# Kernel tuning notes

Measured on AMD Instinct MI355X. Metric: run time of the kernel, lower is better.

Reference implementation:

```python
import jax, jax.numpy as jnp
import numpy as np

B, N, M, D, H = 2, 256, 64, 768, 12
HD = D // H  # head dim 64


def setup_inputs() -> dict:
    key = jax.random.key(0)
    ks = jax.random.split(key, 8)
    s = 0.02
    return {
        "x": jax.random.normal(ks[0], (B, N, D), jnp.float32),
        "sim_embeddings": jax.random.normal(ks[1], (B, N, M, D), jnp.float32),
        "Wq": jax.random.normal(ks[2], (D, D), jnp.float32) * s,
        "bq": jnp.zeros((D,), jnp.float32),
        "Wkv": jax.random.normal(ks[3], (D, 2 * D), jnp.float32) * s,
        "bkv": jnp.zeros((2 * D,), jnp.float32),
        "Wp": jax.random.normal(ks[4], (D, D), jnp.float32) * s,
        "bp": jnp.zeros((D,), jnp.float32),
    }


def reference(x, sim_embeddings, Wq, bq, Wkv, bkv, Wp, bp):
    # x: (B,N,D); sim_embeddings: (B,N,M,D)
    b, n, d = x.shape
    m = sim_embeddings.shape[2]
    scale = HD ** -0.5

    q = (x @ Wq + bq).reshape(b, n, H, HD).transpose(0, 2, 1, 3)  # (B,H,N,hd)

    kv_x = x @ Wkv + bkv                       # (B,N,2D)
    k_x, v_x = jnp.split(kv_x, 2, axis=-1)
    k_x = k_x.reshape(b, n, H, HD).transpose(0, 2, 1, 3)  # (B,H,N,hd) shared-global K
    v_x = v_x.reshape(b, n, H, HD).transpose(0, 2, 1, 3)

    kv_s = sim_embeddings @ Wkv + bkv          # (B,N,M,2D)
    k_s, v_s = jnp.split(kv_s, 2, axis=-1)
    k_s = k_s.reshape(b, n, m, H, HD).transpose(0, 3, 1, 2, 4)  # (B,H,N,M,hd) per-query local K
    v_s = v_s.reshape(b, n, m, H, HD).transpose(0, 3, 1, 2, 4)

    # scores over concatenated [global N keys | local M keys] without expanding K to (B,N,N+M,D)
    sg = jnp.einsum('bhnd,bhkd->bhnk', q, k_x) * scale   # (B,H,N,N)
    sl = jnp.einsum('bhnd,bhnmd->bhnm', q, k_s) * scale  # (B,H,N,M)
    attn = jax.nn.softmax(jnp.concatenate([sg, sl], axis=-1), axis=-1)
    ag, al = attn[..., :n], attn[..., n:]

    out = (jnp.einsum('bhnk,bhkd->bhnd', ag, v_x)
           + jnp.einsum('bhnm,bhnmd->bhnd', al, v_s))   # (B,H,N,hd)
    out = out.transpose(0, 2, 1, 3).reshape(b, n, d)
    return out @ Wp + bp
```

## Files before the change

kernel.cpp:

```cpp
#include <hip/hip_runtime.h>
#include <stdint.h>

#define DEV_INLINE __device__ __forceinline__

typedef __bf16 bf16x8 __attribute__((ext_vector_type(8)));
typedef float f32x4 __attribute__((ext_vector_type(4)));

typedef const __attribute__((address_space(1))) void* gas_ptr;
typedef __attribute__((address_space(3))) void* las_ptr;

DEV_INLINE unsigned short f2bf(float f) {
    union { __bf16 h; unsigned short u; } v;
    v.h = (__bf16)f;
    return v.u;
}

template <int N> DEV_INLINE void waitcnt_vm() {
    asm volatile("s_waitcnt vmcnt(%0)" :: "n"(N) : "memory");
}
DEV_INLINE void hard_barrier() {
    __builtin_amdgcn_sched_barrier(0);
    __builtin_amdgcn_s_barrier();
    __builtin_amdgcn_sched_barrier(0);
}

__global__ __launch_bounds__(256)
void prep_all_kernel(const float* __restrict__ x, unsigned short* __restrict__ xb,
                     const float* __restrict__ Wkv, unsigned short* __restrict__ wkvb,
                     const float* __restrict__ bq, const float* __restrict__ bkv,
                     float* __restrict__ bias1, float* __restrict__ zbuf,
                     const float* __restrict__ Wq, const float* __restrict__ Wp,
                     unsigned short* __restrict__ w1t, unsigned short* __restrict__ wpt) {
    __shared__ float tl[64][65];
    const int bid = blockIdx.x, t = threadIdx.x;
    if (bid < 1536) {
        const float* s; unsigned short* d; long i;
        if (bid < 384) { s = x;   d = xb;   i = (long)bid * 256 + t; }
        else           { s = Wkv; d = wkvb; i = (long)(bid - 384) * 256 + t; }
        float4 a = ((const float4*)s)[i];
        ushort4 o;
        o.x = f2bf(a.x); o.y = f2bf(a.y); o.z = f2bf(a.z); o.w = f2bf(a.w);
        ((ushort4*)d)[i] = o;
    } else if (bid < 1548) {
        int i = (bid - 1536) * 256 + t;
        if (i < 768) bias1[i] = bq[i];
        else if (i < 2304) bias1[i] = bkv[i - 768];
        else zbuf[i - 2304] = 0.f;
    } else {
        int tb = bid - 1548;
        int bx = tb % 48, by = tb / 48;
        const float* src; unsigned short* dst; int C;
        if (bx < 12)      { src = Wq;  dst = w1t;              C = 768; }
        else if (bx < 36) { src = Wkv; dst = w1t + 768L * 768; C = 1536; bx -= 12; }
        else              { src = Wp;  dst = wpt;              C = 768; bx -= 36; }
        int c0 = bx * 64, r0 = by * 64;
        int tx = t & 63, ty = t >> 6;
        #pragma unroll
        for (int i = 0; i < 64; i += 4)
            tl[ty + i][tx] = src[(long)(r0 + ty + i) * C + c0 + tx];
        __syncthreads();
        #pragma unroll
        for (int i = 0; i < 64; i += 4)
            dst[(long)(c0 + ty + i) * 768 + r0 + tx] = f2bf(tl[tx][ty + i]);
    }
}

template <int WM, int WN, int WAVES_M, bool G1E>
DEV_INLINE void gemm_body(const unsigned short* A, int lda,
                          const unsigned short* BT, int ldb,
                          const unsigned short* A2, int lda2,
                          const unsigned short* B2, int ldb2, int K1,
                          const float* bias, void* Cout, int ldc, int K,
                          const float* cin, int OUT, long obase, long tm, long tn,
                          unsigned short* As, unsigned short* Bs,
                          float* g1_qf, unsigned short* g1_qb,
                          unsigned short* g1_kxb, unsigned short* g1_vxT) {
    constexpr int TR = WAVES_M * WM * 16;
    constexpr int TC = (4 / WAVES_M) * WN * 16;
    constexpr int NL = TR / 32 + TC / 32;
    const int tid = threadIdx.x;
    const int w = tid >> 6, lane = tid & 63;
    const int lm = lane & 15, quad = lane >> 4;
    const int m_off = (w % WAVES_M) * WM * 16;
    const int n_off = (w / WAVES_M) * WN * 16;
    const int lrow8 = lane >> 3;
    const int lcol_sw = (((lane & 7) ^ lrow8) * 8);

    f32x4 acc[WM][WN];
    #pragma unroll
    for (int mi = 0; mi < WM; ++mi)
        #pragma unroll
        for (int ni = 0; ni < WN; ++ni) acc[mi][ni] = f32x4{0.f, 0.f, 0.f, 0.f};

    auto stage = [&](int k0, int pb) {
        const unsigned short* Ab; const unsigned short* Bb;
        int la, lb, kc;
        if (k0 < K1) { Ab = A;  Bb = BT; la = lda;  lb = ldb;  kc = k0; }
        else         { Ab = A2; Bb = B2; la = lda2; lb = ldb2; kc = k0 - K1; }
        unsigned short* Asb = As + pb * (TR * 64);
        unsigned short* Bsb = Bs + pb * (TC * 64);
        #pragma unroll
        for (int i = 0; i < TR / 32; ++i) {
            int rr = w * (TR / 4) + i * 8;
            const unsigned short* ga = Ab + (tm + rr + lrow8) * la + kc + lcol_sw;
            __builtin_amdgcn_global_load_lds((gas_ptr)ga, (las_ptr)(Asb + rr * 64), 16, 0, 0);
        }
        #pragma unroll
        for (int i = 0; i < TC / 32; ++i) {
            int rr = w * (TC / 4) + i * 8;
            const unsigned short* gb = Bb + (tn + rr + lrow8) * lb + kc + lcol_sw;
            __builtin_amdgcn_global_load_lds((gas_ptr)gb, (las_ptr)(Bsb + rr * 64), 16, 0, 0);
        }
    };

    stage(0, 0);
    const int nt = K >> 6;
    for (int t = 0; t < nt; ++t) {
        const int cur = t & 1;
        if (t + 1 < nt) {
            stage((t + 1) << 6, cur ^ 1);
            waitcnt_vm<NL>();
        } else {
            waitcnt_vm<0>();
        }
        hard_barrier();
        const unsigned short* Asb = As + cur * (TR * 64);
        const unsigned short* Bsb = Bs + cur * (TC * 64);
        #pragma unroll
        for (int kk = 0; kk < 2; ++kk) {
            bf16x8 af[WM], bfr[WN];
            #pragma unroll
            for (int mi = 0; mi < WM; ++mi) {
                int r = m_off + mi * 16 + lm;
                af[mi] = *(const bf16x8*)(Asb + r * 64 + (((kk * 4 + quad) ^ (r & 7)) * 8));
            }
            #pragma unroll
            for (int ni = 0; ni < WN; ++ni) {
                int r = n_off + ni * 16 + lm;
                bfr[ni] = *(const bf16x8*)(Bsb + r * 64 + (((kk * 4 + quad) ^ (r & 7)) * 8));
            }
            #pragma unroll
            for (int mi = 0; mi < WM; ++mi)
                #pragma unroll
                for (int ni = 0; ni < WN; ++ni)
                    acc[mi][ni] = __builtin_amdgcn_mfma_f32_16x16x32_bf16(
                        af[mi], bfr[ni], acc[mi][ni], 0, 0, 0);
        }
        hard_barrier();
    }

    #pragma unroll
    for (int mi = 0; mi < WM; ++mi) {
        #pragma unroll
        for (int ni = 0; ni < WN; ++ni) {
            long col = tn + n_off + ni * 16 + lm;
            float bv = bias[col];
            #pragma unroll
            for (int r = 0; r < 4; ++r) {
                long row = tm + m_off + mi * 16 + quad * 4 + r;
                float v = acc[mi][ni][r] + bv;
                if (G1E) {
                    if (col < 768) {
                        g1_qf[row * 768 + col] = v;
                        g1_qb[row * 768 + col] = f2bf(v);
                    } else if (col < 1536) {
                        g1_kxb[row * 768 + (col - 768)] = f2bf(v);
                    } else {
                        int j = (int)col - 1536, h = j >> 6, d = j & 63;
                        int bb = (int)row >> 8, nn = (int)row & 255;
                        g1_vxT[((long)(bb * 12 + h) * 64 + d) * 256 + nn] = f2bf(v);
                    }
                } else {
                    long idx = obase + row * ldc + col;
                    if (cin) v += cin[idx];
                    if (OUT == 0) ((float*)Cout)[idx] = v;
                    else ((unsigned short*)Cout)[idx] = f2bf(v);
                }
            }
        }
    }
}

template <int WM, int WN, int WAVES_M, bool G1E>
__global__ __launch_bounds__(256)
void gemm_bf16_kernel(const unsigned short* __restrict__ A, int lda,
                      const unsigned short* __restrict__ BT, int ldb,
                      const float* __restrict__ bias,
                      void* __restrict__ Cout, int ldc, int K,
                      const float* __restrict__ cin, int OUT,
                      long aZb, long aZh, long bZb, long bZh, long oZb, long oZh,
                      float* __restrict__ g1_qf, unsigned short* __restrict__ g1_qb,
                      unsigned short* __restrict__ g1_kxb,
                      unsigned short* __restrict__ g1_vxT) {
    constexpr int TR = WAVES_M * WM * 16;
    constexpr int TC = (4 / WAVES_M) * WN * 16;
    __shared__ unsigned short As[2 * TR * 64];
    __shared__ unsigned short Bs[2 * TC * 64];
    const int z = blockIdx.z, zb = z / 12, zh = z % 12;
    gemm_body<WM, WN, WAVES_M, G1E>(
        A + zb * aZb + zh * aZh, lda, BT + zb * bZb + zh * bZh, ldb,
        nullptr, 0, nullptr, 0, 1 << 30,
        bias, Cout, ldc, K, cin, OUT, zb * oZb + zh * oZh,
        (long)blockIdx.y * TR, (long)blockIdx.x * TC, As, Bs,
        g1_qf, g1_qb, g1_kxb, g1_vxT);
}

__global__ __launch_bounds__(256)
void gemm_qwsg_kernel(const unsigned short* __restrict__ qb,
                      const unsigned short* __restrict__ wkvb,
                      const unsigned short* __restrict__ kxb,
                      const float* __restrict__ zbuf,
                      unsigned short* __restrict__ qWb,
                      float* __restrict__ sgbuf) {
    __shared__ unsigned short As[2 * 64 * 64];
    __shared__ unsigned short Bs[2 * 64 * 64];
    int bid = blockIdx.x;
    if (bid < 1152) {
        int bx = bid % 12, by = (bid / 12) % 8, h = bid / 96;
        gemm_body<2, 2, 2, false>(
            qb + h * 64, 768, wkvb + h * 64, 1536,
            nullptr, 0, nullptr, 0, 1 << 30,
            zbuf, qWb, 768, 64, nullptr, 1, (long)h * 393216,
            (long)by * 64, (long)bx * 64, As, Bs,
            nullptr, nullptr, nullptr, nullptr);
    } else {
        int bid2 = bid - 1152;
        int bx = bid2 % 4, by = (bid2 / 4) % 4, z = bid2 / 16;
        int zb = z / 12, zh = z % 12;
        gemm_body<2, 2, 2, false>(
            qb + zb * 196608 + zh * 64, 768, kxb + zb * 196608 + zh * 64, 768,
            nullptr, 0, nullptr, 0, 1 << 30,
            zbuf, sgbuf, 256, 64, nullptr, 0,
            (long)zb * 786432 + (long)zh * 65536,
            (long)by * 64, (long)bx * 64, As, Bs,
            nullptr, nullptr, nullptr, nullptr);
    }
}

template <int WM, int WN, int WAVES_M>
__global__ __launch_bounds__(256)
void gemm_concat_kernel(const unsigned short* __restrict__ A, int lda, long aZb, long aZh,
                        const unsigned short* __restrict__ BT, int ldb, long bZb, long bZh,
                        const unsigned short* __restrict__ A2, int lda2, long a2Zb, long a2Zh,
                        const unsigned short* __restrict__ B2, int ldb2, long b2Zb, long b2Zh,
                        int K1, int K, const float* __restrict__ bias,
                        void* __restrict__ Cout, int ldc,
                        const float* __restrict__ cin, int OUT, long oZb, long oZh) {
    constexpr int TR = WAVES_M * WM * 16;
    constexpr int TC = (4 / WAVES_M) * WN * 16;
    __shared__ unsigned short As[2 * TR * 64];
    __shared__ unsigned short Bs[2 * TC * 64];
    const int z = blockIdx.z, zb = z / 12, zh = z % 12;
    gemm_body<WM, WN, WAVES_M, false>(
        A + zb * aZb + zh * aZh, lda, BT + zb * bZb + zh * bZh, ldb,
        A2 + zb * a2Zb + zh * a2Zh, lda2, B2 + zb * b2Zb + zh * b2Zh, ldb2, K1,
        bias, Cout, ldc, K, cin, OUT, zb * oZb + zh * oZh,
        (long)blockIdx.y * TR, (long)blockIdx.x * TC, As, Bs,
        nullptr, nullptr, nullptr, nullptr);
}

__global__ __launch_bounds__(512)
void attn_mega_kernel(const float* __restrict__ sim,
                      const unsigned short* __restrict__ qWb,
                      const float* __restrict__ qf,
                      const float* __restrict__ bkv,
                      const float* __restrict__ sgbuf,
                      unsigned short* __restrict__ agb,
                      float* __restrict__ outg0,
                      unsigned short* __restrict__ simbar) {
    __shared__ unsigned short sim_s[12 * 64 * 64];
    __shared__ unsigned short qw_s[16 * 784];
    __shared__ float scl[2][12][68];
    __shared__ float al_s[12][64];
    __shared__ float slb_s[12];

    const int t = threadIdx.x;
    const int lane = t & 63, w = t >> 6;
    const int lm = lane & 15, quad = lane >> 4;
    const int n_ = blockIdx.x;
    const int b = n_ >> 8, n = n_ & 255;
    const float* simn = sim + (long)n_ * 49152;

    #pragma unroll
    for (int g3 = 0; g3 < 3; ++g3) {
        float4 va[4], vb[4]; int dso[4];
        #pragma unroll
        for (int i = 0; i < 4; ++i) {
            int j = t + 512 * (g3 * 4 + i);
            int r = j / 96, rem = j - r * 96;
            int c = rem >> 3, q8 = rem & 7;
            const float* gp = simn + r * 768 + c * 64 + q8 * 8;
            va[i] = *(const float4*)gp;
            vb[i] = *(const float4*)(gp + 4);
            dso[i] = c * 4096 + r * 64 + ((q8 ^ (r & 7)) * 8);
        }
        #pragma unroll
        for (int i = 0; i < 4; ++i) {
            union { bf16x8 v; unsigned short u[8]; } pk;
            pk.u[0] = f2bf(va[i].x); pk.u[1] = f2bf(va[i].y);
            pk.u[2] = f2bf(va[i].z); pk.u[3] = f2bf(va[i].w);
            pk.u[4] = f2bf(vb[i].x); pk.u[5] = f2bf(vb[i].y);
            pk.u[6] = f2bf(vb[i].z); pk.u[7] = f2bf(vb[i].w);
            *(bf16x8*)(sim_s + dso[i]) = pk.v;
        }
    }

    #pragma unroll
    for (int rep = 0; rep < 2; ++rep) {
        int i = t + rep * 512;
        int h = i / 96, cc = i - h * 96;
        *(bf16x8*)(qw_s + h * 784 + cc * 8) =
            *(const bf16x8*)(qWb + ((long)h * 512 + n_) * 768 + cc * 8);
    }
    if (t < 128) {
        int i = t + 1024;
        int h = i / 96, cc = i - h * 96;
        *(bf16x8*)(qw_s + h * 784 + cc * 8) =
            *(const bf16x8*)(qWb + ((long)h * 512 + n_) * 768 + cc * 8);
    }
    if (t < 392) *(bf16x8*)(qw_s + 12 * 784 + t * 8) = bf16x8{};

    if (t < 256) {
        float p0 = qf[(long)n_ * 768 + t] * bkv[t];
        float p1 = qf[(long)n_ * 768 + t + 256] * bkv[t + 256];
        float p2 = qf[(long)n_ * 768 + t + 512] * bkv[t + 512];
        #pragma unroll
        for (int off = 32; off > 0; off >>= 1) {
            p0 += __shfl_xor(p0, off);
            p1 += __shfl_xor(p1, off);
            p2 += __shfl_xor(p2, off);
        }
        if (lane == 0) { slb_s[w] = p0; slb_s[w + 4] = p1; slb_s[w + 8] = p2; }
    }
    __syncthreads();

    {
        const int mb = w & 3, kh = w >> 2;
        f32x4 acc = {};
        const int r = mb * 16 + lm;
        #pragma unroll
        for (int cc = 0; cc < 6; ++cc) {
            const int c = kh * 6 + cc;
            #pragma unroll
            for (int kk = 0; kk < 2; ++kk) {
                bf16x8 af = *(const bf16x8*)(sim_s + c * 4096 + r * 64 +
                                             (((kk * 4 + quad) ^ (r & 7)) * 8));
                bf16x8 bfr = *(const bf16x8*)(qw_s + lm * 784 + c * 64 + kk * 32 + quad * 8);
                acc = __builtin_amdgcn_mfma_f32_16x16x32_bf16(af, bfr, acc, 0, 0, 0);
            }
        }
        if (lm < 12) {
            #pragma unroll
            for (int r2 = 0; r2 < 4; ++r2)
                scl[kh][lm][mb * 16 + quad * 4 + r2] = acc[r2];
        }
    }
    __syncthreads();

    if (w < 6) {
        #pragma unroll
        for (int i = 0; i < 2; ++i) {
            const int h = w * 2 + i;
            const float* sgr = sgbuf + (long)(b * 12 + h) * 65536 + (long)n * 256;
            float v0 = sgr[lane] * 0.125f, v1 = sgr[lane + 64] * 0.125f,
                  v2 = sgr[lane + 128] * 0.125f, v3 = sgr[lane + 192] * 0.125f;
            float v4 = (scl[0][h][lane] + scl[1][h][lane] + slb_s[h]) * 0.125f;
            float mx = fmaxf(fmaxf(fmaxf(v0, v1), fmaxf(v2, v3)), v4);
            #pragma unroll
            for (int off = 32; off > 0; off >>= 1) mx = fmaxf(mx, __shfl_xor(mx, off));
            float e0 = __expf(v0 - mx), e1 = __expf(v1 - mx), e2 = __expf(v2 - mx),
                  e3 = __expf(v3 - mx), e4 = __expf(v4 - mx);
            float s = e0 + e1 + e2 + e3 + e4;
            #pragma unroll
            for (int off = 32; off > 0; off >>= 1) s += __shfl_xor(s, off);
            float inv = __frcp_rn(s);
            unsigned short* agr = agb + (long)(b * 12 + h) * 65536 + (long)n * 256;
            agr[lane] = f2bf(e0 * inv); agr[lane + 64] = f2bf(e1 * inv);
            agr[lane + 128] = f2bf(e2 * inv); agr[lane + 192] = f2bf(e3 * inv);
            float al = e4 * inv;
            al_s[h][lane] = al;
            float am = al;
            #pragma unroll
            for (int off = 32; off > 0; off >>= 1) am += __shfl_xor(am, off);
            outg0[(long)n_ * 768 + h * 64 + lane] = am * bkv[768 + h * 64 + lane];
        }
    }
    __syncthreads();

    {
        float a[12];
        #pragma unroll
        for (int h = 0; h < 12; ++h) a[h] = 0.f;
        #pragma unroll 4
        for (int m = 0; m < 64; ++m) {
            float s = simn[(long)m * 768 + t];
            #pragma unroll
            for (int h = 0; h < 12; ++h) a[h] += al_s[h][m] * s;
        }
        #pragma unroll
        for (int h = 0; h < 12; ++h)
            simbar[((long)h * 512 + n_) * 768 + t] = f2bf(a[h]);
    }
    if (t < 256) {
        float a[12];
        #pragma unroll
        for (int h = 0; h < 12; ++h) a[h] = 0.f;
        #pragma unroll 4
        for (int m = 0; m < 64; ++m) {
            float s = simn[(long)m * 768 + 512 + t];
            #pragma unroll
            for (int h = 0; h < 12; ++h) a[h] += al_s[h][m] * s;
        }
        #pragma unroll
        for (int h = 0; h < 12; ++h)
            simbar[((long)h * 512 + n_) * 768 + 512 + t] = f2bf(a[h]);
    }
}


extern "C" void kernel_launch(void* const* d_in, const int* in_sizes, int n_in,
                              void* d_out, int out_size, void* d_ws, size_t ws_size,
                              hipStream_t stream) {
    const float* x   = (const float*)d_in[0];
    const float* sim = (const float*)d_in[1];
    const float* Wq  = (const float*)d_in[2];
    const float* bq  = (const float*)d_in[3];
    const float* Wkv = (const float*)d_in[4];
    const float* bkv = (const float*)d_in[5];
    const float* Wp  = (const float*)d_in[6];
    const float* bp  = (const float*)d_in[7];
    float* out = (float*)d_out;

    char* ws = (char*)d_ws;
    size_t off = 0;
    auto alloc = [&](size_t bytes) {
        char* p = ws + off;
        off += (bytes + 255) & ~(size_t)255;
        return p;
    };
    unsigned short* xb     = (unsigned short*)alloc(512UL * 768 * 2);
    unsigned short* w1t    = (unsigned short*)alloc(2304UL * 768 * 2);
    unsigned short* wkvb   = (unsigned short*)alloc(768UL * 1536 * 2);
    unsigned short* wpt    = (unsigned short*)alloc(768UL * 768 * 2);
    float*          qf     = (float*)alloc(512UL * 768 * 4);
    unsigned short* qb     = (unsigned short*)alloc(512UL * 768 * 2);
    unsigned short* kxb    = (unsigned short*)alloc(512UL * 768 * 2);
    unsigned short* vxT    = (unsigned short*)alloc(24UL * 64 * 256 * 2);
    unsigned short* qWb    = (unsigned short*)alloc(12UL * 512 * 768 * 2);
    float*          sgbuf  = (float*)alloc(24UL * 65536 * 4);
    unsigned short* agb    = (unsigned short*)alloc(24UL * 65536 * 2);
    float*          outg0  = (float*)alloc(512UL * 768 * 4);
    unsigned short* simbar = (unsigned short*)alloc(12UL * 512 * 768 * 2);
    unsigned short* attnb  = (unsigned short*)alloc(512UL * 768 * 2);
    float*          bias1  = (float*)alloc(2304UL * 4);
    float*          zbuf   = (float*)alloc(768UL * 4);

    prep_all_kernel<<<2124, 256, 0, stream>>>(
        x, xb, Wkv, wkvb, bq, bkv, bias1, zbuf, Wq, Wp, w1t, wpt);

    gemm_bf16_kernel<1, 2, 2, true><<<dim3(36, 16, 1), 256, 0, stream>>>(
        xb, 768, w1t, 768, bias1, nullptr, 768, 768, nullptr, 0,
        0, 0, 0, 0, 0, 0, qf, qb, kxb, vxT);

    gemm_qwsg_kernel<<<1536, 256, 0, stream>>>(qb, wkvb, kxb, zbuf, qWb, sgbuf);

    attn_mega_kernel<<<512, 512, 0, stream>>>(
        sim, qWb, qf, bkv, sgbuf, agb, outg0, simbar);

    gemm_concat_kernel<1, 1, 2><<<dim3(2, 8, 24), 256, 0, stream>>>(
        simbar, 768, 196608, 393216,
        w1t + 1536L * 768, 768, 0, 49152,
        agb, 256, 786432, 65536,
        vxT, 256, 196608, 16384,
        768, 1024, zbuf, attnb, 768, outg0, 1, 196608, 64);

    gemm_bf16_kernel<1, 1, 2, false><<<dim3(24, 16, 1), 256, 0, stream>>>(
        attnb, 768, wpt, 768, bp, out, 768, 768, nullptr, 0,
        0, 0, 0, 0, 0, 0, nullptr, nullptr, nullptr, nullptr);
}
```

Measured before the change: 242.1 us.

## Split attention mega-kernel into bf16 sim prepass, pipelined local-score kernel, and attn2

The fp32 sim_embeddings tensor is converted to bf16 in the prep kernel. A new kernel computes local scores from that bf16 copy, staging chunks into LDS with double-buffered global_load_lds. The softmax and weighted-sum step moves into a separate kernel over a (512,3) grid, so each block handles a third of the columns. The aim is to raise occupancy by dropping the large 96KB+ shared-memory footprint and to overlap loads with MFMA, at the cost of an extra full pass over sim (fp32 read, bf16 write) and softmax recomputed three times per row.

```diff
diff --git a/kernel.cpp b/kernel.cpp
--- a/kernel.cpp
+++ b/kernel.cpp
@@ -30,9 +30,22 @@
                      const float* __restrict__ bq, const float* __restrict__ bkv,
                      float* __restrict__ bias1, float* __restrict__ zbuf,
                      const float* __restrict__ Wq, const float* __restrict__ Wp,
-                     unsigned short* __restrict__ w1t, unsigned short* __restrict__ wpt) {
+                     unsigned short* __restrict__ w1t, unsigned short* __restrict__ wpt,
+                     const float* __restrict__ sim, unsigned short* __restrict__ simb) {
     __shared__ float tl[64][65];
     const int bid = blockIdx.x, t = threadIdx.x;
+    if (bid >= 2124) {
+        long i = (long)(bid - 2124) * 256 + t;
+        const float4* sp = (const float4*)sim + i * 2;
+        float4 a = sp[0], b = sp[1];
+        union { bf16x8 v; unsigned short u[8]; } pk;
+        pk.u[0] = f2bf(a.x); pk.u[1] = f2bf(a.y);
+        pk.u[2] = f2bf(a.z); pk.u[3] = f2bf(a.w);
+        pk.u[4] = f2bf(b.x); pk.u[5] = f2bf(b.y);
+        pk.u[6] = f2bf(b.z); pk.u[7] = f2bf(b.w);
+        ((bf16x8*)simb)[i] = pk.v;
+        return;
+    }
     if (bid < 1536) {
         const float* s; unsigned short* d; long i;
         if (bid < 384) { s = x;   d = xb;   i = (long)bid * 256 + t; }
@@ -259,68 +272,83 @@
         nullptr, nullptr, nullptr, nullptr);
 }
 
-__global__ __launch_bounds__(512)
-void attn_mega_kernel(const float* __restrict__ sim,
-                      const unsigned short* __restrict__ qWb,
-                      const float* __restrict__ qf,
-                      const float* __restrict__ bkv,
-                      const float* __restrict__ sgbuf,
-                      unsigned short* __restrict__ agb,
-                      float* __restrict__ outg0,
-                      unsigned short* __restrict__ simbar) {
-    __shared__ unsigned short sim_s[12 * 64 * 64];
+__global__ __launch_bounds__(256)
+void slpart2_kernel(const unsigned short* __restrict__ simb,
+                    const unsigned short* __restrict__ qWb,
+                    float* __restrict__ sclp) {
     __shared__ unsigned short qw_s[16 * 784];
-    __shared__ float scl[2][12][68];
+    __shared__ unsigned short ss[2][64 * 64];
+    const int t = threadIdx.x;
+    const int w = t >> 6, lane = t & 63;
+    const int lm = lane & 15, quad = lane >> 4;
+    const int lrow8 = lane >> 3;
+    const int lcol_sw = ((lane & 7) ^ lrow8) * 8;
+    const int n_ = blockIdx.x;
+    const unsigned short* simn = simb + (long)n_ * 49152;
+
+    auto stage = [&](int c, int pb) {
+        unsigned short* dst = ss[pb];
+        #pragma unroll
+        for (int i = 0; i < 2; ++i) {
+            int rr = w * 16 + i * 8;
+            const unsigned short* ga = simn + (rr + lrow8) * 768 + c * 64 + lcol_sw;
+            __builtin_amdgcn_global_load_lds((gas_ptr)ga, (las_ptr)(dst + rr * 64), 16, 0, 0);
+        }
+    };
+    stage(0, 0);
+
+    for (int idx = t; idx < 1152; idx += 256) {
+        int h = idx / 96, c = idx - h * 96;
+        *(bf16x8*)(qw_s + h * 784 + c * 8) =
+            *(const bf16x8*)(qWb + ((long)h * 512 + n_) * 768 + c * 8);
+    }
+    __syncthreads();
+
+    f32x4 acc = {};
+    const int r = w * 16 + lm;
+    for (int c = 0; c < 12; ++c) {
+        const int cur = c & 1;
+        if (c + 1 < 12) {
+            stage(c + 1, cur ^ 1);
+            waitcnt_vm<2>();
+        } else {
+            waitcnt_vm<0>();
+        }
+        hard_barrier();
+        const unsigned short* buf = ss[cur];
+        #pragma unroll
+        for (int kk = 0; kk < 2; ++kk) {
+            bf16x8 af = *(const bf16x8*)(buf + r * 64 + (((kk * 4 + quad) ^ (r & 7)) * 8));
+            bf16x8 bfr = *(const bf16x8*)(qw_s + lm * 784 + c * 64 + kk * 32 + quad * 8);
+            acc = __builtin_amdgcn_mfma_f32_16x16x32_bf16(af, bfr, acc, 0, 0, 0);
+        }
+        hard_barrier();
+    }
+    if (lm < 12) {
+        float* dst = sclp + ((long)n_ * 12 + lm) * 64 + w * 16 + quad * 4;
+        #pragma unroll
+        for (int r2 = 0; r2 < 4; ++r2) dst[r2] = acc[r2];
+    }
+}
+
+__global__ __launch_bounds__(256)
+void attn2_kernel(const float* __restrict__ sim,
+                  const float* __restrict__ qf,
+                  const float* __restrict__ bkv,
+                  const float* __restrict__ sclp,
+                  const float* __restrict__ sgbuf,
+                  unsigned short* __restrict__ agb,
+                  float* __restrict__ outg0,
+                  unsigned short* __restrict__ simbar) {
+    __shared__ float slb_s[12];
     __shared__ float al_s[12][64];
-    __shared__ float slb_s[12];
-
     const int t = threadIdx.x;
     const int lane = t & 63, w = t >> 6;
-    const int lm = lane & 15, quad = lane >> 4;
-    const int n_ = blockIdx.x;
+    const int n_ = blockIdx.x, cg = blockIdx.y;
     const int b = n_ >> 8, n = n_ & 255;
     const float* simn = sim + (long)n_ * 49152;
 
-    #pragma unroll
-    for (int g3 = 0; g3 < 3; ++g3) {
-        float4 va[4], vb[4]; int dso[4];
-        #pragma unroll
-        for (int i = 0; i < 4; ++i) {
-            int j = t + 512 * (g3 * 4 + i);
-            int r = j / 96, rem = j - r * 96;
-            int c = rem >> 3, q8 = rem & 7;
-            const float* gp = simn + r * 768 + c * 64 + q8 * 8;
-            va[i] = *(const float4*)gp;
-            vb[i] = *(const float4*)(gp + 4);
-            dso[i] = c * 4096 + r * 64 + ((q8 ^ (r & 7)) * 8);
-        }
-        #pragma unroll
-        for (int i = 0; i < 4; ++i) {
-            union { bf16x8 v; unsigned short u[8]; } pk;
-            pk.u[0] = f2bf(va[i].x); pk.u[1] = f2bf(va[i].y);
-            pk.u[2] = f2bf(va[i].z); pk.u[3] = f2bf(va[i].w);
-            pk.u[4] = f2bf(vb[i].x); pk.u[5] = f2bf(vb[i].y);
-            pk.u[6] = f2bf(vb[i].z); pk.u[7] = f2bf(vb[i].w);
-            *(bf16x8*)(sim_s + dso[i]) = pk.v;
-        }
-    }
-
-    #pragma unroll
-    for (int rep = 0; rep < 2; ++rep) {
-        int i = t + rep * 512;
-        int h = i / 96, cc = i - h * 96;
-        *(bf16x8*)(qw_s + h * 784 + cc * 8) =
-            *(const bf16x8*)(qWb + ((long)h * 512 + n_) * 768 + cc * 8);
-    }
-    if (t < 128) {
-        int i = t + 1024;
-        int h = i / 96, cc = i - h * 96;
-        *(bf16x8*)(qw_s + h * 784 + cc * 8) =
-            *(const bf16x8*)(qWb + ((long)h * 512 + n_) * 768 + cc * 8);
-    }
-    if (t < 392) *(bf16x8*)(qw_s + 12 * 784 + t * 8) = bf16x8{};
-
-    if (t < 256) {
+    {
         float p0 = qf[(long)n_ * 768 + t] * bkv[t];
         float p1 = qf[(long)n_ * 768 + t + 256] * bkv[t + 256];
         float p2 = qf[(long)n_ * 768 + t + 512] * bkv[t + 512];
@@ -334,51 +362,28 @@
     }
     __syncthreads();
 
-    {
-        const int mb = w & 3, kh = w >> 2;
-        f32x4 acc = {};
-        const int r = mb * 16 + lm;
-        #pragma unroll
-        for (int cc = 0; cc < 6; ++cc) {
-            const int c = kh * 6 + cc;
-            #pragma unroll
-            for (int kk = 0; kk < 2; ++kk) {
-                bf16x8 af = *(const bf16x8*)(sim_s + c * 4096 + r * 64 +
-                                             (((kk * 4 + quad) ^ (r & 7)) * 8));
-                bf16x8 bfr = *(const bf16x8*)(qw_s + lm * 784 + c * 64 + kk * 32 + quad * 8);
-                acc = __builtin_amdgcn_mfma_f32_16x16x32_bf16(af, bfr, acc, 0, 0, 0);
-            }
-        }
-        if (lm < 12) {
-            #pragma unroll
-            for (int r2 = 0; r2 < 4; ++r2)
-                scl[kh][lm][mb * 16 + quad * 4 + r2] = acc[r2];
-        }
-    }
-    __syncthreads();
-
-    if (w < 6) {
-        #pragma unroll
-        for (int i = 0; i < 2; ++i) {
-            const int h = w * 2 + i;
-            const float* sgr = sgbuf + (long)(b * 12 + h) * 65536 + (long)n * 256;
-            float v0 = sgr[lane] * 0.125f, v1 = sgr[lane + 64] * 0.125f,
-                  v2 = sgr[lane + 128] * 0.125f, v3 = sgr[lane + 192] * 0.125f;
-            float v4 = (scl[0][h][lane] + scl[1][h][lane] + slb_s[h]) * 0.125f;
-            float mx = fmaxf(fmaxf(fmaxf(v0, v1), fmaxf(v2, v3)), v4);
-            #pragma unroll
-            for (int off = 32; off > 0; off >>= 1) mx = fmaxf(mx, __shfl_xor(mx, off));
-            float e0 = __expf(v0 - mx), e1 = __expf(v1 - mx), e2 = __expf(v2 - mx),
-                  e3 = __expf(v3 - mx), e4 = __expf(v4 - mx);
-            float s = e0 + e1 + e2 + e3 + e4;
-            #pragma unroll
-            for (int off = 32; off > 0; off >>= 1) s += __shfl_xor(s, off);
-            float inv = __frcp_rn(s);
+    #pragma unroll
+    for (int i = 0; i < 3; ++i) {
+        const int h = w * 3 + i;
+        const float* sgr = sgbuf + (long)(b * 12 + h) * 65536 + (long)n * 256;
+        float v0 = sgr[lane] * 0.125f, v1 = sgr[lane + 64] * 0.125f,
+              v2 = sgr[lane + 128] * 0.125f, v3 = sgr[lane + 192] * 0.125f;
+        float v4 = (sclp[((long)n_ * 12 + h) * 64 + lane] + slb_s[h]) * 0.125f;
+        float mx = fmaxf(fmaxf(fmaxf(v0, v1), fmaxf(v2, v3)), v4);
+        #pragma unroll
+        for (int off = 32; off > 0; off >>= 1) mx = fmaxf(mx, __shfl_xor(mx, off));
+        float e0 = __expf(v0 - mx), e1 = __expf(v1 - mx), e2 = __expf(v2 - mx),
+              e3 = __expf(v3 - mx), e4 = __expf(v4 - mx);
+        float s = e0 + e1 + e2 + e3 + e4;
+        #pragma unroll
+        for (int off = 32; off > 0; off >>= 1) s += __shfl_xor(s, off);
+        float inv = __frcp_rn(s);
+        float al = e4 * inv;
+        al_s[h][lane] = al;
+        if (cg == 0) {
             unsigned short* agr = agb + (long)(b * 12 + h) * 65536 + (long)n * 256;
             agr[lane] = f2bf(e0 * inv); agr[lane + 64] = f2bf(e1 * inv);
             agr[lane + 128] = f2bf(e2 * inv); agr[lane + 192] = f2bf(e3 * inv);
-            float al = e4 * inv;
-            al_s[h][lane] = al;
             float am = al;
             #pragma unroll
             for (int off = 32; off > 0; off >>= 1) am += __shfl_xor(am, off);
@@ -387,34 +392,19 @@
     }
     __syncthreads();
 
-    {
-        float a[12];
-        #pragma unroll
-        for (int h = 0; h < 12; ++h) a[h] = 0.f;
-        #pragma unroll 4
-        for (int m = 0; m < 64; ++m) {
-            float s = simn[(long)m * 768 + t];
-            #pragma unroll
-            for (int h = 0; h < 12; ++h) a[h] += al_s[h][m] * s;
-        }
-        #pragma unroll
-        for (int h = 0; h < 12; ++h)
-            simbar[((long)h * 512 + n_) * 768 + t] = f2bf(a[h]);
-    }
-    if (t < 256) {
-        float a[12];
-        #pragma unroll
-        for (int h = 0; h < 12; ++h) a[h] = 0.f;
-        #pragma unroll 4
-        for (int m = 0; m < 64; ++m) {
-            float s = simn[(long)m * 768 + 512 + t];
-            #pragma unroll
-            for (int h = 0; h < 12; ++h) a[h] += al_s[h][m] * s;
-        }
-        #pragma unroll
-        for (int h = 0; h < 12; ++h)
-            simbar[((long)h * 512 + n_) * 768 + 512 + t] = f2bf(a[h]);
-    }
+    const int c = cg * 256 + t;
+    float a[12];
+    #pragma unroll
+    for (int h = 0; h < 12; ++h) a[h] = 0.f;
+    #pragma unroll 4
+    for (int m = 0; m < 64; ++m) {
+        float s = simn[(long)m * 768 + c];
+        #pragma unroll
+        for (int h = 0; h < 12; ++h) a[h] += al_s[h][m] * s;
+    }
+    #pragma unroll
+    for (int h = 0; h < 12; ++h)
+        simbar[((long)h * 512 + n_) * 768 + c] = f2bf(a[h]);
 }
 
 
@@ -447,16 +437,18 @@
     unsigned short* kxb    = (unsigned short*)alloc(512UL * 768 * 2);
     unsigned short* vxT    = (unsigned short*)alloc(24UL * 64 * 256 * 2);
     unsigned short* qWb    = (unsigned short*)alloc(12UL * 512 * 768 * 2);
+    unsigned short* simb   = (unsigned short*)alloc(512UL * 64 * 768 * 2);
     float*          sgbuf  = (float*)alloc(24UL * 65536 * 4);
     unsigned short* agb    = (unsigned short*)alloc(24UL * 65536 * 2);
     float*          outg0  = (float*)alloc(512UL * 768 * 4);
+    float*          sclp   = (float*)alloc(512UL * 12 * 64 * 4);
     unsigned short* simbar = (unsigned short*)alloc(12UL * 512 * 768 * 2);
     unsigned short* attnb  = (unsigned short*)alloc(512UL * 768 * 2);
     float*          bias1  = (float*)alloc(2304UL * 4);
     float*          zbuf   = (float*)alloc(768UL * 4);
 
-    prep_all_kernel<<<2124, 256, 0, stream>>>(
-        x, xb, Wkv, wkvb, bq, bkv, bias1, zbuf, Wq, Wp, w1t, wpt);
+    prep_all_kernel<<<14412, 256, 0, stream>>>(
+        x, xb, Wkv, wkvb, bq, bkv, bias1, zbuf, Wq, Wp, w1t, wpt, sim, simb);
 
     gemm_bf16_kernel<1, 2, 2, true><<<dim3(36, 16, 1), 256, 0, stream>>>(
         xb, 768, w1t, 768, bias1, nullptr, 768, 768, nullptr, 0,
@@ -464,8 +456,10 @@
 
     gemm_qwsg_kernel<<<1536, 256, 0, stream>>>(qb, wkvb, kxb, zbuf, qWb, sgbuf);
 
-    attn_mega_kernel<<<512, 512, 0, stream>>>(
-        sim, qWb, qf, bkv, sgbuf, agb, outg0, simbar);
+    slpart2_kernel<<<512, 256, 0, stream>>>(simb, qWb, sclp);
+
+    attn2_kernel<<<dim3(512, 3), 256, 0, stream>>>(
+        sim, qf, bkv, sclp, sgbuf, agb, outg0, simbar);
 
     gemm_concat_kernel<1, 1, 2><<<dim3(2, 8, 24), 256, 0, stream>>>(
         simbar, 768, 196608, 393216,
```

Result: no change. 246.6 us (+1.9%).
